# Kernel tuning notes

Measured on AMD Instinct MI355X. Metric: run time of the kernel, lower is better.

## Reference

```python
import jax, jax.numpy as jnp
import numpy as np

N_HEADS = 16


def _rope(x, sin, cos):
    # x: [B, H, T, D]; sin/cos: [1, 1, T, D]
    x1 = x[..., ::2]
    x2 = x[..., 1::2]
    xr = jnp.stack((-x2, x1), axis=-1).reshape(x.shape)
    return x * cos + xr * sin


def setup_inputs() -> dict:
    key = jax.random.key(0)
    k_x, k_s, k_c, k_w1, k_w2 = jax.random.split(key, 5)
    B, T, C = 4, 2048, 2048
    hd = C // N_HEADS
    x = jax.random.normal(k_x, (B, T, C), dtype=jnp.float32)
    sin = jax.random.uniform(k_s, (1, 1, T, hd), dtype=jnp.float32)
    cos = jax.random.uniform(k_c, (1, 1, T, hd), dtype=jnp.float32)
    W_qkv = jax.random.normal(k_w1, (C, 3 * C), dtype=jnp.float32) * 0.02
    W_proj = jax.random.normal(k_w2, (C, C), dtype=jnp.float32) * 0.02
    return {"x": x, "sin": sin, "cos": cos, "W_qkv": W_qkv, "W_proj": W_proj}


def reference(x, sin, cos, W_qkv, W_proj):
    B, T, C = x.shape
    hd = C // N_HEADS
    qkv = x @ W_qkv  # [B, T, 3C]
    q, k, v = jnp.split(qkv, 3, axis=-1)
    # [B, T, C] -> [B, H, T, D]
    q = q.reshape(B, T, N_HEADS, hd).transpose(0, 2, 1, 3)
    k = k.reshape(B, T, N_HEADS, hd).transpose(0, 2, 1, 3)
    v = v.reshape(B, T, N_HEADS, hd).transpose(0, 2, 1, 3)
    q = _rope(q, sin[:, :, :T, :], cos[:, :, :T, :])
    k = _rope(k, sin[:, :, :T, :], cos[:, :, :T, :])
    scale = 1.0 / jnp.sqrt(jnp.asarray(hd, dtype=x.dtype))
    scores = jnp.einsum("bhqd,bhkd->bhqk", q, k) * scale
    causal = jnp.tril(jnp.ones((T, T), dtype=bool))
    scores = jnp.where(causal, scores, jnp.asarray(-jnp.inf, dtype=scores.dtype))
    attn = jax.nn.softmax(scores, axis=-1)
    y = jnp.einsum("bhqk,bhkd->bhqd", attn, v)  # [B, H, T, D]
    y = y.transpose(0, 2, 1, 3).reshape(B, T, C)
    return y @ W_proj
```

## Files before the change

### kernel.cpp

```cpp
#include <hip/hip_runtime.h>
#include <hip/hip_bf16.h>
#include <stdint.h>

typedef uint32_t u32;
typedef uint16_t u16;
typedef __attribute__((ext_vector_type(8))) short short8;
typedef __attribute__((ext_vector_type(4))) float floatx4;

#define NH 16
#define HD 128
#define TSEQ 2048
#define NB 4
#define CM 2048
#define MROWS (NB*TSEQ)
#define NQKV (3*CM)

__device__ __forceinline__ u16 f2bf(float f) {
    union { float f; u32 u; } v; v.f = f;
    return (u16)((v.u + 0x7fffu + ((v.u >> 16) & 1u)) >> 16);
}

__device__ __forceinline__ void gll16(u16* lds, const u16* g) {
    __builtin_amdgcn_global_load_lds((const __attribute__((address_space(1))) void*)g,
                                     (__attribute__((address_space(3))) void*)lds,
                                     16, 0, 0);
}

__global__ __launch_bounds__(256) void convert_x_kernel(const float* __restrict__ in,
                                                        u16* __restrict__ out) {
    int idx = (blockIdx.x * 256 + threadIdx.x) * 8;
    float4 a = *(const float4*)(in + idx);
    float4 b = *(const float4*)(in + idx + 4);
    union { u16 s[8]; uint4 v; } o;
    o.s[0] = f2bf(a.x); o.s[1] = f2bf(a.y); o.s[2] = f2bf(a.z); o.s[3] = f2bf(a.w);
    o.s[4] = f2bf(b.x); o.s[5] = f2bf(b.y); o.s[6] = f2bf(b.z); o.s[7] = f2bf(b.w);
    *(uint4*)(out + idx) = o.v;
}

__global__ __launch_bounds__(256) void transpose_bf_kernel(const float* __restrict__ in,
                                                           u16* __restrict__ out,
                                                           int R, int Cn) {
    __shared__ float tile[32][33];
    int tx = threadIdx.x, ty = threadIdx.y;
    int c0 = blockIdx.x * 32, r0 = blockIdx.y * 32;
#pragma unroll
    for (int i = 0; i < 4; i++)
        tile[ty + i * 8][tx] = in[(size_t)(r0 + ty + i * 8) * Cn + c0 + tx];
    __syncthreads();
#pragma unroll
    for (int i = 0; i < 4; i++)
        out[(size_t)(c0 + ty + i * 8) * R + r0 + tx] = f2bf(tile[tx][ty + i * 8]);
}

__global__ __launch_bounds__(256, 2) void gemm_qkv_rope(const u16* __restrict__ A,
                                                        const u16* __restrict__ BT,
                                                        const float* __restrict__ sinp,
                                                        const float* __restrict__ cosp,
                                                        u16* __restrict__ q_ws,
                                                        u16* __restrict__ k_ws,
                                                        u16* __restrict__ v_ws) {
    __shared__ u16 As[4096];
    __shared__ u16 Bs[4096];
    int tid = threadIdx.x;
    int w = tid >> 6, lane = tid & 63, quad = lane >> 4, l15 = lane & 15;
    int mw = (w >> 1) * 64, nw = (w & 1) * 64;
    int rowBase = blockIdx.y * 128;
    int colBase = blockIdx.x * 128;

    floatx4 acc[4][4];
#pragma unroll
    for (int mi = 0; mi < 4; mi++)
#pragma unroll
        for (int ni = 0; ni < 4; ni++) acc[mi][ni] = (floatx4){0.f, 0.f, 0.f, 0.f};

    const u16* Ag0 = A + (size_t)(rowBase + lane) * CM + w * 8;
    const u16* Ag1 = A + (size_t)(rowBase + 64 + lane) * CM + w * 8;
    const u16* Bg0 = BT + (size_t)(colBase + lane) * CM + w * 8;
    const u16* Bg1 = BT + (size_t)(colBase + 64 + lane) * CM + w * 8;
    u16* AsW = &As[w * 1024];
    u16* BsW = &Bs[w * 1024];

    for (int k0 = 0; k0 < CM; k0 += 32) {
        __syncthreads();
        gll16(AsW, Ag0 + k0);
        gll16(AsW + 512, Ag1 + k0);
        gll16(BsW, Bg0 + k0);
        gll16(BsW + 512, Bg1 + k0);
        __syncthreads();
        short8 af[4], bf[4];
#pragma unroll
        for (int mi = 0; mi < 4; mi++)
            af[mi] = *(const short8*)(&As[quad * 1024 + (mw + mi * 16 + l15) * 8]);
#pragma unroll
        for (int ni = 0; ni < 4; ni++)
            bf[ni] = *(const short8*)(&Bs[quad * 1024 + (nw + ni * 16 + l15) * 8]);
#pragma unroll
        for (int mi = 0; mi < 4; mi++)
#pragma unroll
            for (int ni = 0; ni < 4; ni++)
                acc[mi][ni] = __builtin_amdgcn_mfma_f32_16x16x32_bf16(af[mi], bf[ni],
                                                                      acc[mi][ni], 0, 0, 0);
    }

    const float inv_sqrt_hd = 0.08838834764831845f;
#pragma unroll
    for (int mi = 0; mi < 4; mi++) {
#pragma unroll
        for (int ni = 0; ni < 4; ni++) {
            int j = colBase + nw + ni * 16 + l15;
            int sec = j >> 11;
            int jj = j & 2047;
            int h = jj >> 7, d = jj & 127;
            if (sec == 2) {
                int r0 = rowBase + mw + mi * 16 + quad * 4;
                int b = r0 >> 11, t0 = r0 & 2047;
                union { u16 s[4]; uint2 v; } pk;
#pragma unroll
                for (int reg = 0; reg < 4; reg++) pk.s[reg] = f2bf(acc[mi][ni][reg]);
                *(uint2*)(&v_ws[((size_t)(b * NH + h) * HD + d) * TSEQ + t0]) = pk.v;
            } else {
#pragma unroll
                for (int reg = 0; reg < 4; reg++) {
                    int r = rowBase + mw + mi * 16 + quad * 4 + reg;
                    int b = r >> 11, t = r & 2047;
                    float v = acc[mi][ni][reg];
                    float partner = __shfl_xor(v, 1, 64);
                    size_t dsti = (size_t)((b * NH + h) * TSEQ + t) * HD + d;
                    float s = sinp[t * HD + d], c = cosp[t * HD + d];
                    float o = v * c + ((d & 1) ? partner * s : -partner * s);
                    if (sec == 0) o *= inv_sqrt_hd;
                    ((sec == 0) ? q_ws : k_ws)[dsti] = f2bf(o);
                }
            }
        }
    }
}

__global__ __launch_bounds__(256, 2) void attn_kernel(const u16* __restrict__ q_ws,
                                                      const u16* __restrict__ k_ws,
                                                      const u16* __restrict__ vt_ws,
                                                      u16* __restrict__ y_bf) {
    __shared__ u16 Ks[16 * 512];
    __shared__ u16 Vt[8 * 1024];
    __shared__ u16 Ps[128 * 72];
    int tid = threadIdx.x;
    int w = tid >> 6, lane = tid & 63, quad = lane >> 4, l15 = lane & 15;
    int qt = 15 - (blockIdx.x >> 6);
    int bh = blockIdx.x & 63;
    int b = bh >> 4, h = bh & 15;
    const u16* Qg = q_ws + (size_t)bh * TSEQ * HD;
    const u16* Kg = k_ws + (size_t)bh * TSEQ * HD;
    const u16* Vg = vt_ws + (size_t)bh * HD * TSEQ;

    short8 qf[2][4];
#pragma unroll
    for (int mi = 0; mi < 2; mi++)
#pragma unroll
        for (int kk = 0; kk < 4; kk++)
            qf[mi][kk] = *(const short8*)(&Qg[(size_t)(qt * 128 + w * 32 + mi * 16 + l15) * HD +
                                              kk * 32 + quad * 8]);

    floatx4 O[2][8];
#pragma unroll
    for (int mi = 0; mi < 2; mi++)
#pragma unroll
        for (int f = 0; f < 8; f++) O[mi][f] = (floatx4){0.f, 0.f, 0.f, 0.f};
    float l_i[2][4];
#pragma unroll
    for (int mi = 0; mi < 2; mi++)
#pragma unroll
        for (int g = 0; g < 4; g++) l_i[mi][g] = 0.f;

    int ktmax = 2 * qt + 1;
    for (int kt = 0; kt <= ktmax; kt++) {
        const u16* Ktg = Kg + (size_t)(kt * 64) * HD;
        const u16* Vtg = Vg + kt * 64;
        __syncthreads();
#pragma unroll
        for (int j = 0; j < 4; j++) {
            int s = 4 * w + j;
            gll16(&Ks[s * 512], Ktg + (size_t)lane * HD + s * 8);
        }
#pragma unroll
        for (int j = 0; j < 4; j++) {
            int s = 2 * w + (j >> 1), hh = j & 1;
            gll16(&Vt[s * 1024 + hh * 512], Vtg + (size_t)(hh * 64 + lane) * TSEQ + s * 8);
        }
        __syncthreads();

        floatx4 S[2][4];
#pragma unroll
        for (int nf = 0; nf < 4; nf++) {
            short8 bb[4];
#pragma unroll
            for (int kk = 0; kk < 4; kk++)
                bb[kk] = *(const short8*)(&Ks[(kk * 4 + quad) * 512 + (nf * 16 + l15) * 8]);
#pragma unroll
            for (int mi = 0; mi < 2; mi++) {
                floatx4 a4 = (floatx4){0.f, 0.f, 0.f, 0.f};
#pragma unroll
                for (int kk = 0; kk < 4; kk++)
                    a4 = __builtin_amdgcn_mfma_f32_16x16x32_bf16(qf[mi][kk], bb[kk], a4, 0, 0, 0);
                S[mi][nf] = a4;
            }
        }
        if (kt >= 2 * qt) {
#pragma unroll
            for (int mi = 0; mi < 2; mi++)
#pragma unroll
                for (int nf = 0; nf < 4; nf++) {
                    int key = kt * 64 + nf * 16 + l15;
#pragma unroll
                    for (int reg = 0; reg < 4; reg++) {
                        int query = qt * 128 + w * 32 + mi * 16 + quad * 4 + reg;
                        if (key > query) S[mi][nf][reg] = -1e4f;
                    }
                }
        }
#pragma unroll
        for (int mi = 0; mi < 2; mi++)
#pragma unroll
            for (int nf = 0; nf < 4; nf++)
#pragma unroll
                for (int reg = 0; reg < 4; reg++) {
                    float p = __expf(S[mi][nf][reg]);
                    l_i[mi][reg] += p;
                    Ps[(w * 32 + mi * 16 + quad * 4 + reg) * 72 + nf * 16 + l15] = f2bf(p);
                }
        short8 pa[2][2];
#pragma unroll
        for (int mi = 0; mi < 2; mi++)
#pragma unroll
            for (int kk = 0; kk < 2; kk++)
                pa[mi][kk] = *(const short8*)(&Ps[(w * 32 + mi * 16 + l15) * 72 +
                                                  kk * 32 + quad * 8]);
#pragma unroll
        for (int f = 0; f < 8; f++) {
            short8 vb[2];
#pragma unroll
            for (int kk = 0; kk < 2; kk++)
                vb[kk] = *(const short8*)(&Vt[(kk * 4 + quad) * 1024 + (f * 16 + l15) * 8]);
#pragma unroll
            for (int mi = 0; mi < 2; mi++)
#pragma unroll
                for (int kk = 0; kk < 2; kk++)
                    O[mi][f] = __builtin_amdgcn_mfma_f32_16x16x32_bf16(pa[mi][kk], vb[kk],
                                                                       O[mi][f], 0, 0, 0);
        }
    }

    float inv[2][4];
#pragma unroll
    for (int mi = 0; mi < 2; mi++)
#pragma unroll
        for (int reg = 0; reg < 4; reg++) {
            float l = l_i[mi][reg];
#pragma unroll
            for (int off = 1; off < 16; off <<= 1) l += __shfl_xor(l, off, 64);
            inv[mi][reg] = 1.0f / l;
        }
#pragma unroll
    for (int mi = 0; mi < 2; mi++)
#pragma unroll
        for (int f = 0; f < 8; f++)
#pragma unroll
            for (int reg = 0; reg < 4; reg++) {
                int t = qt * 128 + w * 32 + mi * 16 + quad * 4 + reg;
                int col = h * HD + f * 16 + l15;
                y_bf[(size_t)(b * TSEQ + t) * CM + col] = f2bf(O[mi][f][reg] * inv[mi][reg]);
            }
}

__global__ __launch_bounds__(256, 2) void gemm_proj(const u16* __restrict__ A,
                                                    const u16* __restrict__ BT,
                                                    float* __restrict__ out) {
    __shared__ u16 As[4096];
    __shared__ u16 Bs[4096];
    int tid = threadIdx.x;
    int w = tid >> 6, lane = tid & 63, quad = lane >> 4, l15 = lane & 15;
    int mw = (w >> 1) * 64, nw = (w & 1) * 64;
    int rowBase = blockIdx.y * 128;
    int colBase = blockIdx.x * 128;

    floatx4 acc[4][4];
#pragma unroll
    for (int mi = 0; mi < 4; mi++)
#pragma unroll
        for (int ni = 0; ni < 4; ni++) acc[mi][ni] = (floatx4){0.f, 0.f, 0.f, 0.f};

    const u16* Ag0 = A + (size_t)(rowBase + lane) * CM + w * 8;
    const u16* Ag1 = A + (size_t)(rowBase + 64 + lane) * CM + w * 8;
    const u16* Bg0 = BT + (size_t)(colBase + lane) * CM + w * 8;
    const u16* Bg1 = BT + (size_t)(colBase + 64 + lane) * CM + w * 8;
    u16* AsW = &As[w * 1024];
    u16* BsW = &Bs[w * 1024];

    for (int k0 = 0; k0 < CM; k0 += 32) {
        __syncthreads();
        gll16(AsW, Ag0 + k0);
        gll16(AsW + 512, Ag1 + k0);
        gll16(BsW, Bg0 + k0);
        gll16(BsW + 512, Bg1 + k0);
        __syncthreads();
        short8 af[4], bf[4];
#pragma unroll
        for (int mi = 0; mi < 4; mi++)
            af[mi] = *(const short8*)(&As[quad * 1024 + (mw + mi * 16 + l15) * 8]);
#pragma unroll
        for (int ni = 0; ni < 4; ni++)
            bf[ni] = *(const short8*)(&Bs[quad * 1024 + (nw + ni * 16 + l15) * 8]);
#pragma unroll
        for (int mi = 0; mi < 4; mi++)
#pragma unroll
            for (int ni = 0; ni < 4; ni++)
                acc[mi][ni] = __builtin_amdgcn_mfma_f32_16x16x32_bf16(af[mi], bf[ni],
                                                                      acc[mi][ni], 0, 0, 0);
    }

#pragma unroll
    for (int mi = 0; mi < 4; mi++) {
#pragma unroll
        for (int ni = 0; ni < 4; ni++) {
            int j = colBase + nw + ni * 16 + l15;
#pragma unroll
            for (int reg = 0; reg < 4; reg++) {
                int r = rowBase + mw + mi * 16 + quad * 4 + reg;
                out[(size_t)r * CM + j] = acc[mi][ni][reg];
            }
        }
    }
}

extern "C" void kernel_launch(void* const* d_in, const int* in_sizes, int n_in,
                              void* d_out, int out_size, void* d_ws, size_t ws_size,
                              hipStream_t stream) {
    const float* x      = (const float*)d_in[0];
    const float* sinp   = (const float*)d_in[1];
    const float* cosp   = (const float*)d_in[2];
    const float* W_qkv  = (const float*)d_in[3];
    const float* W_proj = (const float*)d_in[4];
    float* out = (float*)d_out;

    char* ws = (char*)d_ws;
    size_t off = 0;
    u16* x_bf   = (u16*)(ws + off); off += (size_t)MROWS * CM * 2;
    u16* wqkvT  = (u16*)(ws + off); off += (size_t)NQKV * CM * 2;
    u16* wprojT = (u16*)(ws + off); off += (size_t)CM * CM * 2;
    u16* q_ws   = (u16*)(ws + off); off += (size_t)MROWS * CM * 2;
    u16* k_ws   = (u16*)(ws + off); off += (size_t)MROWS * CM * 2;
    u16* v_ws   = (u16*)(ws + off); off += (size_t)MROWS * CM * 2;
    u16* y_bf   = x_bf;

    convert_x_kernel<<<(MROWS * CM) / (256 * 8), 256, 0, stream>>>(x, x_bf);
    transpose_bf_kernel<<<dim3(NQKV / 32, CM / 32), dim3(32, 8), 0, stream>>>(W_qkv, wqkvT, CM, NQKV);
    transpose_bf_kernel<<<dim3(CM / 32, CM / 32), dim3(32, 8), 0, stream>>>(W_proj, wprojT, CM, CM);
    gemm_qkv_rope<<<dim3(NQKV / 128, MROWS / 128), 256, 0, stream>>>(x_bf, wqkvT, sinp, cosp,
                                                                     q_ws, k_ws, v_ws);
    attn_kernel<<<(TSEQ / 128) * 64, 256, 0, stream>>>(q_ws, k_ws, v_ws, y_bf);
    gemm_proj<<<dim3(CM / 128, MROWS / 128), 256, 0, stream>>>(y_bf, wprojT, out);
}
```

Baseline: 819.8 us.

## Register-prefetch next tiles, pad LDS rows, remap GEMM blocks per XCD

Replaces direct global-to-LDS loads with register prefetch of the next K tile in both GEMMs and the attention kernel. Global loads for the next iteration now overlap the MFMA work on the current one. The GEMMs also switch to a row-major LDS layout padded to 40 elements per row to avoid bank conflicts. They use a 1D grid with an XCD-aware block mapping so that blocks sharing A rows land on the same XCD for L2 reuse. The costs are extra registers, an LDS store round-trip, and reliance on the 8-XCD round-robin dispatch assumption.

```diff
diff --git a/kernel.cpp b/kernel.cpp
--- a/kernel.cpp
+++ b/kernel.cpp
@@ -18,12 +18,6 @@
 __device__ __forceinline__ u16 f2bf(float f) {
     union { float f; u32 u; } v; v.f = f;
     return (u16)((v.u + 0x7fffu + ((v.u >> 16) & 1u)) >> 16);
-}
-
-__device__ __forceinline__ void gll16(u16* lds, const u16* g) {
-    __builtin_amdgcn_global_load_lds((const __attribute__((address_space(1))) void*)g,
-                                     (__attribute__((address_space(3))) void*)lds,
-                                     16, 0, 0);
 }
 
 __global__ __launch_bounds__(256) void convert_x_kernel(const float* __restrict__ in,
@@ -59,13 +53,15 @@
                                                         u16* __restrict__ q_ws,
                                                         u16* __restrict__ k_ws,
                                                         u16* __restrict__ v_ws) {
-    __shared__ u16 As[4096];
-    __shared__ u16 Bs[4096];
+    __shared__ u16 As[128 * 40];
+    __shared__ u16 Bs[128 * 40];
     int tid = threadIdx.x;
     int w = tid >> 6, lane = tid & 63, quad = lane >> 4, l15 = lane & 15;
     int mw = (w >> 1) * 64, nw = (w & 1) * 64;
-    int rowBase = blockIdx.y * 128;
-    int colBase = blockIdx.x * 128;
+    int blk = blockIdx.x;
+    int xcd = blk & 7, idx8 = blk >> 3;
+    int rowBase = (xcd * 8 + (idx8 & 7)) * 128;
+    int colBase = (idx8 >> 3) * 128;
 
     floatx4 acc[4][4];
 #pragma unroll
@@ -73,27 +69,36 @@
 #pragma unroll
         for (int ni = 0; ni < 4; ni++) acc[mi][ni] = (floatx4){0.f, 0.f, 0.f, 0.f};
 
-    const u16* Ag0 = A + (size_t)(rowBase + lane) * CM + w * 8;
-    const u16* Ag1 = A + (size_t)(rowBase + 64 + lane) * CM + w * 8;
-    const u16* Bg0 = BT + (size_t)(colBase + lane) * CM + w * 8;
-    const u16* Bg1 = BT + (size_t)(colBase + 64 + lane) * CM + w * 8;
-    u16* AsW = &As[w * 1024];
-    u16* BsW = &Bs[w * 1024];
+    int r0s = tid >> 2, c8s = (tid & 3) * 8;
+    int r1s = (tid + 256) >> 2;
+    const u16* Arow0 = A + (size_t)(rowBase + r0s) * CM + c8s;
+    const u16* Arow1 = A + (size_t)(rowBase + r1s) * CM + c8s;
+    const u16* Brow0 = BT + (size_t)(colBase + r0s) * CM + c8s;
+    const u16* Brow1 = BT + (size_t)(colBase + r1s) * CM + c8s;
+
+    uint4 pa0 = *(const uint4*)(Arow0), pa1 = *(const uint4*)(Arow1);
+    uint4 pb0 = *(const uint4*)(Brow0), pb1 = *(const uint4*)(Brow1);
 
     for (int k0 = 0; k0 < CM; k0 += 32) {
         __syncthreads();
-        gll16(AsW, Ag0 + k0);
-        gll16(AsW + 512, Ag1 + k0);
-        gll16(BsW, Bg0 + k0);
-        gll16(BsW + 512, Bg1 + k0);
+        *(uint4*)(&As[r0s * 40 + c8s]) = pa0;
+        *(uint4*)(&As[r1s * 40 + c8s]) = pa1;
+        *(uint4*)(&Bs[r0s * 40 + c8s]) = pb0;
+        *(uint4*)(&Bs[r1s * 40 + c8s]) = pb1;
+        if (k0 + 32 < CM) {
+            pa0 = *(const uint4*)(Arow0 + k0 + 32);
+            pa1 = *(const uint4*)(Arow1 + k0 + 32);
+            pb0 = *(const uint4*)(Brow0 + k0 + 32);
+            pb1 = *(const uint4*)(Brow1 + k0 + 32);
+        }
         __syncthreads();
         short8 af[4], bf[4];
 #pragma unroll
         for (int mi = 0; mi < 4; mi++)
-            af[mi] = *(const short8*)(&As[quad * 1024 + (mw + mi * 16 + l15) * 8]);
+            af[mi] = *(const short8*)(&As[(mw + mi * 16 + l15) * 40 + quad * 8]);
 #pragma unroll
         for (int ni = 0; ni < 4; ni++)
-            bf[ni] = *(const short8*)(&Bs[quad * 1024 + (nw + ni * 16 + l15) * 8]);
+            bf[ni] = *(const short8*)(&Bs[(nw + ni * 16 + l15) * 40 + quad * 8]);
 #pragma unroll
         for (int mi = 0; mi < 4; mi++)
 #pragma unroll
@@ -171,20 +176,44 @@
 #pragma unroll
         for (int g = 0; g < 4; g++) l_i[mi][g] = 0.f;
 
+    uint4 kreg[4], vreg[4];
+#pragma unroll
+    for (int j = 0; j < 4; j++) {
+        int s = 4 * w + j;
+        kreg[j] = *(const uint4*)(Kg + (size_t)lane * HD + s * 8);
+    }
+#pragma unroll
+    for (int j = 0; j < 4; j++) {
+        int s = 2 * w + (j >> 1), hh = j & 1;
+        vreg[j] = *(const uint4*)(Vg + (size_t)(hh * 64 + lane) * TSEQ + s * 8);
+    }
+
     int ktmax = 2 * qt + 1;
     for (int kt = 0; kt <= ktmax; kt++) {
-        const u16* Ktg = Kg + (size_t)(kt * 64) * HD;
-        const u16* Vtg = Vg + kt * 64;
         __syncthreads();
 #pragma unroll
         for (int j = 0; j < 4; j++) {
             int s = 4 * w + j;
-            gll16(&Ks[s * 512], Ktg + (size_t)lane * HD + s * 8);
+            *(uint4*)(&Ks[s * 512 + lane * 8]) = kreg[j];
         }
 #pragma unroll
         for (int j = 0; j < 4; j++) {
             int s = 2 * w + (j >> 1), hh = j & 1;
-            gll16(&Vt[s * 1024 + hh * 512], Vtg + (size_t)(hh * 64 + lane) * TSEQ + s * 8);
+            *(uint4*)(&Vt[s * 1024 + hh * 512 + lane * 8]) = vreg[j];
+        }
+        if (kt < ktmax) {
+            const u16* Ktg = Kg + (size_t)((kt + 1) * 64) * HD;
+            const u16* Vtg = Vg + (kt + 1) * 64;
+#pragma unroll
+            for (int j = 0; j < 4; j++) {
+                int s = 4 * w + j;
+                kreg[j] = *(const uint4*)(Ktg + (size_t)lane * HD + s * 8);
+            }
+#pragma unroll
+            for (int j = 0; j < 4; j++) {
+                int s = 2 * w + (j >> 1), hh = j & 1;
+                vreg[j] = *(const uint4*)(Vtg + (size_t)(hh * 64 + lane) * TSEQ + s * 8);
+            }
         }
         __syncthreads();
 
@@ -274,13 +303,15 @@
 __global__ __launch_bounds__(256, 2) void gemm_proj(const u16* __restrict__ A,
                                                     const u16* __restrict__ BT,
                                                     float* __restrict__ out) {
-    __shared__ u16 As[4096];
-    __shared__ u16 Bs[4096];
+    __shared__ u16 As[128 * 40];
+    __shared__ u16 Bs[128 * 40];
     int tid = threadIdx.x;
     int w = tid >> 6, lane = tid & 63, quad = lane >> 4, l15 = lane & 15;
     int mw = (w >> 1) * 64, nw = (w & 1) * 64;
-    int rowBase = blockIdx.y * 128;
-    int colBase = blockIdx.x * 128;
+    int blk = blockIdx.x;
+    int xcd = blk & 7, idx8 = blk >> 3;
+    int rowBase = (xcd * 8 + (idx8 & 7)) * 128;
+    int colBase = (idx8 >> 3) * 128;
 
     floatx4 acc[4][4];
 #pragma unroll
@@ -288,27 +319,36 @@
 #pragma unroll
         for (int ni = 0; ni < 4; ni++) acc[mi][ni] = (floatx4){0.f, 0.f, 0.f, 0.f};
 
-    const u16* Ag0 = A + (size_t)(rowBase + lane) * CM + w * 8;
-    const u16* Ag1 = A + (size_t)(rowBase + 64 + lane) * CM + w * 8;
-    const u16* Bg0 = BT + (size_t)(colBase + lane) * CM + w * 8;
-    const u16* Bg1 = BT + (size_t)(colBase + 64 + lane) * CM + w * 8;
-    u16* AsW = &As[w * 1024];
-    u16* BsW = &Bs[w * 1024];
+    int r0s = tid >> 2, c8s = (tid & 3) * 8;
+    int r1s = (tid + 256) >> 2;
+    const u16* Arow0 = A + (size_t)(rowBase + r0s) * CM + c8s;
+    const u16* Arow1 = A + (size_t)(rowBase + r1s) * CM + c8s;
+    const u16* Brow0 = BT + (size_t)(colBase + r0s) * CM + c8s;
+    const u16* Brow1 = BT + (size_t)(colBase + r1s) * CM + c8s;
+
+    uint4 pa0 = *(const uint4*)(Arow0), pa1 = *(const uint4*)(Arow1);
+    uint4 pb0 = *(const uint4*)(Brow0), pb1 = *(const uint4*)(Brow1);
 
     for (int k0 = 0; k0 < CM; k0 += 32) {
         __syncthreads();
-        gll16(AsW, Ag0 + k0);
-        gll16(AsW + 512, Ag1 + k0);
-        gll16(BsW, Bg0 + k0);
-        gll16(BsW + 512, Bg1 + k0);
+        *(uint4*)(&As[r0s * 40 + c8s]) = pa0;
+        *(uint4*)(&As[r1s * 40 + c8s]) = pa1;
+        *(uint4*)(&Bs[r0s * 40 + c8s]) = pb0;
+        *(uint4*)(&Bs[r1s * 40 + c8s]) = pb1;
+        if (k0 + 32 < CM) {
+            pa0 = *(const uint4*)(Arow0 + k0 + 32);
+            pa1 = *(const uint4*)(Arow1 + k0 + 32);
+            pb0 = *(const uint4*)(Brow0 + k0 + 32);
+            pb1 = *(const uint4*)(Brow1 + k0 + 32);
+        }
         __syncthreads();
         short8 af[4], bf[4];
 #pragma unroll
         for (int mi = 0; mi < 4; mi++)
-            af[mi] = *(const short8*)(&As[quad * 1024 + (mw + mi * 16 + l15) * 8]);
+            af[mi] = *(const short8*)(&As[(mw + mi * 16 + l15) * 40 + quad * 8]);
 #pragma unroll
         for (int ni = 0; ni < 4; ni++)
-            bf[ni] = *(const short8*)(&Bs[quad * 1024 + (nw + ni * 16 + l15) * 8]);
+            bf[ni] = *(const short8*)(&Bs[(nw + ni * 16 + l15) * 40 + quad * 8]);
 #pragma unroll
         for (int mi = 0; mi < 4; mi++)
 #pragma unroll
@@ -354,8 +394,8 @@
     convert_x_kernel<<<(MROWS * CM) / (256 * 8), 256, 0, stream>>>(x, x_bf);
     transpose_bf_kernel<<<dim3(NQKV / 32, CM / 32), dim3(32, 8), 0, stream>>>(W_qkv, wqkvT, CM, NQKV);
     transpose_bf_kernel<<<dim3(CM / 32, CM / 32), dim3(32, 8), 0, stream>>>(W_proj, wprojT, CM, CM);
-    gemm_qkv_rope<<<dim3(NQKV / 128, MROWS / 128), 256, 0, stream>>>(x_bf, wqkvT, sinp, cosp,
-                                                                     q_ws, k_ws, v_ws);
+    gemm_qkv_rope<<<(NQKV / 128) * (MROWS / 128), 256, 0, stream>>>(x_bf, wqkvT, sinp, cosp,
+                                                                    q_ws, k_ws, v_ws);
     attn_kernel<<<(TSEQ / 128) * 64, 256, 0, stream>>>(q_ws, k_ws, v_ws, y_bf);
-    gemm_proj<<<dim3(CM / 128, MROWS / 128), 256, 0, stream>>>(y_bf, wprojT, out);
-}
+    gemm_proj<<<(CM / 128) * (MROWS / 128), 256, 0, stream>>>(y_bf, wprojT, out);
+}
```

New measurement: 728.9 us. 1.12x faster.
